# Kernel optimization log

Hardware: AMD Instinct MI355X
Metric: run time of the kernel (lower is better)

Reference implementation:

```python
import jax, jax.numpy as jnp
import numpy as np

DIM = 4096
N_HEADS = 32
N_KV_HEADS = 8
HEAD_DIM = 128
ROPE_THETA = 10000.0
REPEATS = N_HEADS // N_KV_HEADS
SCALE = HEAD_DIM ** -0.5


def rope(x, seq_len, offset):
    # x: [b, h, seq_len, head_dim]; faithful to source: cos/sin from cat((freqs,freqs)),
    # rotate built by interleaved pair swap then flatten.
    d = x.shape[-1]
    inv_freq = 1.0 / (ROPE_THETA ** (jnp.arange(0, d, 2, dtype=jnp.float32) / d))  # [d/2]
    t = jnp.arange(offset, offset + seq_len, dtype=jnp.float32)                    # [L]
    freqs = t[:, None] * inv_freq[None, :]                                         # [L, d/2]
    emb = jnp.concatenate([freqs, freqs], axis=-1)                                 # [L, d]
    cos_emb = jnp.cos(emb)
    sin_emb = jnp.sin(emb)
    x_even = x[..., 0::2]
    x_odd = x[..., 1::2]
    rotate_x = jnp.stack([-x_odd, x_even], axis=-1).reshape(x.shape)
    return x * cos_emb + rotate_x * sin_emb


def setup_inputs() -> dict:
    key = jax.random.key(0)
    k1, k2, k3, k4, k5 = jax.random.split(key, 5)
    b, l = 1, 2048
    s = 0.02
    x = jax.random.normal(k1, (b, l, DIM), dtype=jnp.float32)
    wq = jax.random.normal(k2, (DIM, N_HEADS * HEAD_DIM), dtype=jnp.float32) * s
    wk = jax.random.normal(k3, (DIM, N_KV_HEADS * HEAD_DIM), dtype=jnp.float32) * s
    wv = jax.random.normal(k4, (DIM, N_KV_HEADS * HEAD_DIM), dtype=jnp.float32) * s
    wo = jax.random.normal(k5, (N_HEADS * HEAD_DIM, DIM), dtype=jnp.float32) * s
    return {"x": x, "wq": wq, "wk": wk, "wv": wv, "wo": wo, "seq_len": l}


def reference(x, wq, wk, wv, wo, seq_len):
    b, l, _ = x.shape
    q = (x @ wq).reshape(b, l, N_HEADS, HEAD_DIM).transpose(0, 2, 1, 3)       # [b,H,l,d]
    k = (x @ wk).reshape(b, l, N_KV_HEADS, HEAD_DIM).transpose(0, 2, 1, 3)    # [b,Hk,l,d]
    v = (x @ wv).reshape(b, l, N_KV_HEADS, HEAD_DIM).transpose(0, 2, 1, 3)
    # repeat KV heads to match query heads (GQA)
    k = jnp.repeat(k, REPEATS, axis=1)   # [b,H,l,d]
    v = jnp.repeat(v, REPEATS, axis=1)
    offset = 0  # cache is None
    q = rope(q, seq_len, offset)
    k = rope(k, seq_len, offset)
    scores = jnp.einsum('bhid,bhjd->bhij', q * SCALE, k)
    scores = jax.nn.softmax(scores.astype(jnp.float32), axis=-1).astype(scores.dtype)
    out = jnp.einsum('bhij,bhjd->bhid', scores, v)
    out = out.transpose(0, 2, 1, 3).reshape(b, l, N_HEADS * HEAD_DIM)
    return out @ wo, (k, v)
```

## Files before the change

### kernel.cpp

```cpp
#include <hip/hip_runtime.h>
#include <cstdint>
#include <cstddef>

#define DIM 4096
#define SEQ 2048
#define NH 32
#define NKV 8
#define HD 128
#define QKVN 6144

typedef __bf16 bf16_t;
typedef __bf16 bf16x8 __attribute__((ext_vector_type(8)));
typedef __bf16 bf16x4 __attribute__((ext_vector_type(4)));
typedef __bf16 bf16x2 __attribute__((ext_vector_type(2)));
typedef float f32x4 __attribute__((ext_vector_type(4)));
typedef int int4v __attribute__((ext_vector_type(4)));

__device__ __forceinline__ f32x4 mfma16(bf16x8 a, bf16x8 b, f32x4 c) {
  return __builtin_amdgcn_mfma_f32_16x16x32_bf16(a, b, c, 0, 0, 0);
}

__device__ __forceinline__ void async16(const bf16_t* g, bf16_t* l) {
  __builtin_amdgcn_global_load_lds((__attribute__((address_space(1))) void*)g,
                                   (__attribute__((address_space(3))) void*)l,
                                   16, 0, 0);
}

__device__ __forceinline__ int pack2(float a, float b) {
  bf16x2 h = { (bf16_t)a, (bf16_t)b };
  return __builtin_bit_cast(int, h);
}

#define LGKM0() do { asm volatile("s_waitcnt lgkmcnt(0)" ::: "memory"); \
                     __builtin_amdgcn_sched_barrier(0); } while (0)
#define VMW4() do { asm volatile("s_waitcnt vmcnt(4)" ::: "memory"); \
                    __builtin_amdgcn_sched_barrier(0); } while (0)

__global__ void cast_x(const float* __restrict__ x, bf16_t* __restrict__ xb) {
  int i = blockIdx.x * 256 + threadIdx.x;
  const float4 v = ((const float4*)x)[i];
  bf16x4 o = { (bf16_t)v.x, (bf16_t)v.y, (bf16_t)v.z, (bf16_t)v.w };
  *(bf16x4*)(xb + (size_t)i * 4) = o;
}

__global__ void tcast(const float* __restrict__ src, bf16_t* __restrict__ dst,
                      int Ncols, int Kdim) {
  __shared__ float tile[32][33];
  int n0 = blockIdx.x * 32, k0 = blockIdx.y * 32;
  int tx = threadIdx.x, ty = threadIdx.y;
#pragma unroll
  for (int r = 0; r < 4; r++)
    tile[ty + 8 * r][tx] = src[(size_t)(k0 + ty + 8 * r) * Ncols + n0 + tx];
  __syncthreads();
#pragma unroll
  for (int r = 0; r < 4; r++)
    dst[(size_t)(n0 + ty + 8 * r) * Kdim + k0 + tx] = (bf16_t)tile[tx][ty + 8 * r];
}

__global__ __launch_bounds__(512) void gemm256(const bf16_t* __restrict__ A,
                                               const bf16_t* __restrict__ Bt,
                                               float* __restrict__ C,
                                               float* __restrict__ Cp,
                                               int M, int N, int K, int Kloc) {
  __shared__ bf16_t As[2][16384];
  __shared__ bf16_t Bs[2][16384];
  const int t = threadIdx.x;
  const int lane = t & 63;
  const int l15 = lane & 15, quad = lane >> 4;
  const int w = t >> 6, wm = w >> 2, wn = w & 3;

  const int gx = gridDim.x;
  const int nwg = gx * gridDim.y;
  const int id = blockIdx.y * gx + blockIdx.x;
  const int swz = (id & 7) * (nwg >> 3) + (id >> 3);
  const int bm = (swz / gx) * 256, bn = (swz % gx) * 256;
  const int kbase = blockIdx.z * Kloc;
  float* __restrict__ Cd = blockIdx.z ? Cp : C;

  const int srow = t >> 2;
  const int gcol = ((t & 3) ^ (srow & 3)) << 3;
  const bf16_t* gA = A + (size_t)(bm + srow) * K + kbase + gcol;
  const bf16_t* gB = Bt + (size_t)(bn + srow) * K + kbase + gcol;
  const int ldst = t * 8;

  const int fcol = ((quad ^ (l15 & 3)) << 3);

  f32x4 acc[8][4] = {};
  bf16x8 af[4], bfr[4][2];

  auto stKh = [&](int b2, int s, int kk) {
    async16(gA + kk + s * 32, &As[b2][s * 8192 + ldst]);
    async16(gA + (size_t)128 * K + kk + s * 32, &As[b2][s * 8192 + 4096 + ldst]);
    async16(gB + kk + s * 32, &Bs[b2][s * 8192 + ldst]);
    async16(gB + (size_t)128 * K + kk + s * 32, &Bs[b2][s * 8192 + 4096 + ldst]);
  };

  stKh(0, 0, 0);
  stKh(0, 1, 0);
  VMW4();
  __builtin_amdgcn_s_barrier();

  const int nkt = Kloc >> 6;
  for (int kt = 0; kt < nkt; ++kt) {
    const int b2 = kt & 1, bn2 = b2 ^ 1;
    const int kn = (kt + 1 == nkt) ? 0 : (kt + 1) << 6;

#pragma unroll
    for (int mi = 0; mi < 4; mi++)
      af[mi] = *(const bf16x8*)&As[b2][(wm * 128 + mi * 16 + l15) * 32 + fcol];
#pragma unroll
    for (int ni = 0; ni < 4; ni++)
      bfr[ni][0] = *(const bf16x8*)&Bs[b2][(wn * 64 + ni * 16 + l15) * 32 + fcol];
    stKh(bn2, 0, kn);
    __builtin_amdgcn_s_barrier();
    LGKM0();
    __builtin_amdgcn_s_setprio(1);
#pragma unroll
    for (int mi = 0; mi < 4; mi++)
#pragma unroll
      for (int ni = 0; ni < 4; ni++)
        acc[mi][ni] = mfma16(af[mi], bfr[ni][0], acc[mi][ni]);
    __builtin_amdgcn_s_setprio(0);
    VMW4();
    __builtin_amdgcn_s_barrier();

#pragma unroll
    for (int mi = 0; mi < 4; mi++)
      af[mi] = *(const bf16x8*)&As[b2][8192 + (wm * 128 + mi * 16 + l15) * 32 + fcol];
#pragma unroll
    for (int ni = 0; ni < 4; ni++)
      bfr[ni][1] = *(const bf16x8*)&Bs[b2][8192 + (wn * 64 + ni * 16 + l15) * 32 + fcol];
    stKh(bn2, 1, kn);
    __builtin_amdgcn_s_barrier();
    LGKM0();
    __builtin_amdgcn_s_setprio(1);
#pragma unroll
    for (int mi = 0; mi < 4; mi++)
#pragma unroll
      for (int ni = 0; ni < 4; ni++)
        acc[mi][ni] = mfma16(af[mi], bfr[ni][1], acc[mi][ni]);
    __builtin_amdgcn_s_setprio(0);
    __builtin_amdgcn_s_barrier();

#pragma unroll
    for (int mi = 0; mi < 4; mi++)
      af[mi] = *(const bf16x8*)&As[b2][(wm * 128 + 64 + mi * 16 + l15) * 32 + fcol];
    __builtin_amdgcn_s_barrier();
    LGKM0();
    __builtin_amdgcn_s_setprio(1);
#pragma unroll
    for (int mi = 0; mi < 4; mi++)
#pragma unroll
      for (int ni = 0; ni < 4; ni++)
        acc[mi + 4][ni] = mfma16(af[mi], bfr[ni][0], acc[mi + 4][ni]);
    __builtin_amdgcn_s_setprio(0);
    __builtin_amdgcn_s_barrier();

#pragma unroll
    for (int mi = 0; mi < 4; mi++)
      af[mi] = *(const bf16x8*)&As[b2][8192 + (wm * 128 + 64 + mi * 16 + l15) * 32 + fcol];
    __builtin_amdgcn_s_barrier();
    LGKM0();
    __builtin_amdgcn_s_setprio(1);
#pragma unroll
    for (int mi = 0; mi < 4; mi++)
#pragma unroll
      for (int ni = 0; ni < 4; ni++)
        acc[mi + 4][ni] = mfma16(af[mi], bfr[ni][1], acc[mi + 4][ni]);
    __builtin_amdgcn_s_setprio(0);
    VMW4();
    __builtin_amdgcn_s_barrier();
  }

#pragma unroll
  for (int m8 = 0; m8 < 8; m8++)
#pragma unroll
    for (int ni = 0; ni < 4; ni++) {
      size_t row = (size_t)bm + wm * 128 + (m8 >> 2) * 64 + (m8 & 3) * 16 + quad * 4;
      size_t col = (size_t)bn + wn * 64 + ni * 16 + l15;
#pragma unroll
      for (int r = 0; r < 4; r++)
        Cd[(row + r) * N + col] = acc[m8][ni][r];
    }
  asm volatile("s_waitcnt vmcnt(0)" ::: "memory");
}

__global__ void addf4(float* __restrict__ o, const float* __restrict__ p) {
  int i = blockIdx.x * 256 + threadIdx.x;
  float4 a = ((const float4*)o)[i];
  const float4 b = ((const float4*)p)[i];
  a.x += b.x; a.y += b.y; a.z += b.z; a.w += b.w;
  ((float4*)o)[i] = a;
}

__global__ void rope_scatter(const float* __restrict__ qkv, bf16_t* __restrict__ Qb,
                             bf16_t* __restrict__ Kb, bf16_t* __restrict__ Vt,
                             float* __restrict__ kOut, float* __restrict__ vOut) {
  int idx = blockIdx.x * 256 + threadIdx.x;
  int t = idx / 3072;
  int p = idx - t * 3072;
  const float NEG_L2T_64 = -0.20762050593046f;
  const float SS = 0.08838834764831845f * 1.4426950408889634f;
  if (p < 2048) {
    int hh = p >> 6, pr = p & 63;
    int d0 = pr << 1;
    const float* src = qkv + (size_t)t * QKVN + hh * HD + d0;
    float a = src[0], b = src[1];
    int j0 = d0 & 63, j1 = (d0 + 1) & 63;
    float th0 = (float)t * exp2f((float)j0 * NEG_L2T_64);
    float th1 = (float)t * exp2f((float)j1 * NEG_L2T_64);
    float o0 = (a * cosf(th0) - b * sinf(th0)) * SS;
    float o1 = (b * cosf(th1) + a * sinf(th1)) * SS;
    bf16_t* dst = Qb + ((size_t)hh * SEQ + t) * HD + d0;
    dst[0] = (bf16_t)o0;
    dst[1] = (bf16_t)o1;
  } else if (p < 2560) {
    int q2 = p - 2048;
    int kh = q2 >> 6, pr = q2 & 63;
    int d0 = pr << 1;
    const float* src = qkv + (size_t)t * QKVN + 4096 + kh * HD + d0;
    float a = src[0], b = src[1];
    int j0 = d0 & 63, j1 = (d0 + 1) & 63;
    float th0 = (float)t * exp2f((float)j0 * NEG_L2T_64);
    float th1 = (float)t * exp2f((float)j1 * NEG_L2T_64);
    float o0 = a * cosf(th0) - b * sinf(th0);
    float o1 = b * cosf(th1) + a * sinf(th1);
    bf16_t* dst = Kb + ((size_t)kh * SEQ + t) * HD + d0;
    dst[0] = (bf16_t)o0;
    dst[1] = (bf16_t)o1;
#pragma unroll
    for (int rep = 0; rep < 4; rep++) {
      float* kp = kOut + ((size_t)(kh * 4 + rep) * SEQ + t) * HD + d0;
      kp[0] = o0;
      kp[1] = o1;
    }
  } else {
    int q2 = p - 2560;
    int kh = q2 >> 6, pr = q2 & 63;
    int d0 = pr << 1;
    const float* src = qkv + (size_t)t * QKVN + 5120 + kh * HD + d0;
    float a = src[0], b = src[1];
#pragma unroll
    for (int rep = 0; rep < 4; rep++) {
      float* vp = vOut + ((size_t)(kh * 4 + rep) * SEQ + t) * HD + d0;
      vp[0] = a;
      vp[1] = b;
    }
    int tp = (t & ~31) + ((t & 12) << 1) + (t & 3) + ((t & 16) >> 2);
    Vt[((size_t)kh * HD + d0) * SEQ + tp] = (bf16_t)a;
    Vt[((size_t)kh * HD + d0 + 1) * SEQ + tp] = (bf16_t)b;
  }
}

__global__ __launch_bounds__(512, 2) void attn_kernel(const bf16_t* __restrict__ Qb,
                                                      const bf16_t* __restrict__ Kb,
                                                      const bf16_t* __restrict__ Vt,
                                                      bf16_t* __restrict__ AO) {
  __shared__ bf16_t Ks[2][8192];
  __shared__ bf16_t Vs[2][8192];
  const int h = blockIdx.y, kh = h >> 2;
  const int qbase = blockIdx.x * 256;
  const int w = threadIdx.x >> 6, lane = threadIdx.x & 63;
  const int l15 = lane & 15, quad = lane >> 4;
  const bf16_t* KbH = Kb + (size_t)kh * SEQ * HD;
  const bf16_t* VtH = Vt + (size_t)kh * HD * SEQ;

  bf16x8 qf[2][4];
#pragma unroll
  for (int nq = 0; nq < 2; nq++) {
    const bf16_t* qp = Qb + ((size_t)h * SEQ + qbase + w * 32 + nq * 16 + l15) * HD + quad * 8;
#pragma unroll
    for (int kc = 0; kc < 4; kc++) qf[nq][kc] = *(const bf16x8*)(qp + kc * 32);
  }

  f32x4 acc[8][2] = {};
  float rsum[2] = {0.f, 0.f};

  auto stage = [&](int buf, int kt0) {
    if (w < 4) {
      int kc = w;
#pragma unroll
      for (int kg = 0; kg < 4; kg++) {
        const bf16_t* g = KbH + (size_t)(kt0 + kg * 16 + (lane >> 2)) * HD + kc * 32 + (lane & 3) * 8;
        async16(g, &Ks[buf][kc * 2048 + kg * 512]);
      }
    } else {
      int vi = w - 4, kt = vi >> 1, dg0 = (vi & 1) * 4;
#pragma unroll
      for (int j = 0; j < 4; j++) {
        int dg = dg0 + j;
        const bf16_t* g = VtH + (size_t)(dg * 16 + (lane >> 2)) * SEQ + kt0 + kt * 32 + (lane & 3) * 8;
        async16(g, &Vs[buf][kt * 4096 + dg * 512]);
      }
    }
  };

  stage(0, 0);
  int buf = 0;

  for (int kt0 = 0; kt0 < SEQ; kt0 += 64, buf ^= 1) {
    __syncthreads();
    if (kt0 + 64 < SEQ) stage(buf ^ 1, kt0 + 64);

    f32x4 sacc[4][2] = {};
#pragma unroll
    for (int mi = 0; mi < 4; mi++)
#pragma unroll
      for (int kc = 0; kc < 4; kc++) {
        bf16x8 kf = *(const bf16x8*)(&Ks[buf][(kc * 64 + mi * 16 + l15) * 32 + quad * 8]);
#pragma unroll
        for (int nq = 0; nq < 2; nq++)
          sacc[mi][nq] = mfma16(kf, qf[nq][kc], sacc[mi][nq]);
      }

    int pk[4][2][2];
#pragma unroll
    for (int mi = 0; mi < 4; mi++)
#pragma unroll
      for (int nq = 0; nq < 2; nq++) {
        float p0 = exp2f(sacc[mi][nq][0]);
        float p1 = exp2f(sacc[mi][nq][1]);
        float p2 = exp2f(sacc[mi][nq][2]);
        float p3 = exp2f(sacc[mi][nq][3]);
        rsum[nq] += (p0 + p1) + (p2 + p3);
        pk[mi][nq][0] = pack2(p0, p1);
        pk[mi][nq][1] = pack2(p2, p3);
      }

#pragma unroll
    for (int kt = 0; kt < 2; kt++) {
#pragma unroll
      for (int nq = 0; nq < 2; nq++) {
        int4v dw;
        dw[0] = pk[2 * kt][nq][0];
        dw[1] = pk[2 * kt][nq][1];
        dw[2] = pk[2 * kt + 1][nq][0];
        dw[3] = pk[2 * kt + 1][nq][1];
        bf16x8 pf = __builtin_bit_cast(bf16x8, dw);
#pragma unroll
        for (int dt = 0; dt < 8; dt++) {
          bf16x8 vf = *(const bf16x8*)(&Vs[buf][(kt * 128 + dt * 16 + l15) * 32 + quad * 8]);
          acc[dt][nq] = mfma16(vf, pf, acc[dt][nq]);
        }
      }
    }
  }

#pragma unroll
  for (int nq = 0; nq < 2; nq++) {
    float rs = rsum[nq];
    rs += __shfl_xor(rs, 16);
    rs += __shfl_xor(rs, 32);
    float inv = 1.0f / rs;
    int q = qbase + w * 32 + nq * 16 + l15;
#pragma unroll
    for (int dt = 0; dt < 8; dt++) {
      bf16x4 o = { (bf16_t)(acc[dt][nq][0] * inv), (bf16_t)(acc[dt][nq][1] * inv),
                   (bf16_t)(acc[dt][nq][2] * inv), (bf16_t)(acc[dt][nq][3] * inv) };
      *(bf16x4*)(AO + (size_t)q * DIM + h * HD + dt * 16 + quad * 4) = o;
    }
  }
}

extern "C" void kernel_launch(void* const* d_in, const int* in_sizes, int n_in,
                              void* d_out, int out_size, void* d_ws, size_t ws_size,
                              hipStream_t stream) {
  const float* x = (const float*)d_in[0];
  const float* wq = (const float*)d_in[1];
  const float* wk = (const float*)d_in[2];
  const float* wv = (const float*)d_in[3];
  const float* wo = (const float*)d_in[4];
  float* out = (float*)d_out;
  float* kOut = out + (size_t)SEQ * DIM;
  float* vOut = kOut + (size_t)NH * SEQ * HD;

  char* ws = (char*)d_ws;
  bf16_t* Xb = (bf16_t*)ws;
  bf16_t* WT = (bf16_t*)(ws + 16777216);
  float* Cp1 = (float*)(ws + 16777216);
  float* QKV = (float*)(ws + 67108864);
  bf16_t* WoT = (bf16_t*)(ws + 67108864);
  bf16_t* Qb = (bf16_t*)(ws + 117440512);
  bf16_t* Kb = (bf16_t*)(ws + 134217728);
  bf16_t* Vt = (bf16_t*)(ws + 138412032);
  bf16_t* AO = Xb;

  dim3 tb(32, 8);
  cast_x<<<8192, 256, 0, stream>>>(x, Xb);
  tcast<<<dim3(128, 128), tb, 0, stream>>>(wq, WT, 4096, 4096);
  tcast<<<dim3(32, 128), tb, 0, stream>>>(wk, WT + (size_t)4096 * 4096, 1024, 4096);
  tcast<<<dim3(32, 128), tb, 0, stream>>>(wv, WT + (size_t)5120 * 4096, 1024, 4096);
  gemm256<<<dim3(24, 8, 1), 512, 0, stream>>>(Xb, WT, QKV, nullptr, 2048, 6144, 4096, 4096);
  rope_scatter<<<24576, 256, 0, stream>>>(QKV, Qb, Kb, Vt, kOut, vOut);
  tcast<<<dim3(128, 128), tb, 0, stream>>>(wo, WoT, 4096, 4096);
  attn_kernel<<<dim3(8, 32), 512, 0, stream>>>(Qb, Kb, Vt, AO);
  gemm256<<<dim3(16, 8, 2), 512, 0, stream>>>(AO, WoT, out, Cp1, 2048, 4096, 4096, 2048);
  addf4<<<8192, 256, 0, stream>>>(out, Cp1);
}
```

Measured before the change: 578.8 us.

## Restructure GEMM LDS tiles to full 64-wide K rows with 8-way XOR swizzle

Changes the shared-memory tile layout from two 32-column K-halves to a single 64-column row per tile, staged with one batch of eight async loads per k-step and an 8-way XOR swizzle. Both halves of the B fragments are loaded at once, and the vmcnt waits are retimed so half of the next stage is waited on mid-iteration. The aim is wider contiguous global reads (128B per row) and fewer barrier and wait points per iteration. The risk is that the new swizzle or the partial-wait timing adds bank conflicts or exposes load latency.

```diff
diff --git a/kernel.cpp b/kernel.cpp
--- a/kernel.cpp
+++ b/kernel.cpp
@@ -33,8 +33,12 @@
 
 #define LGKM0() do { asm volatile("s_waitcnt lgkmcnt(0)" ::: "memory"); \
                      __builtin_amdgcn_sched_barrier(0); } while (0)
-#define VMW4() do { asm volatile("s_waitcnt vmcnt(4)" ::: "memory"); \
-                    __builtin_amdgcn_sched_barrier(0); } while (0)
+
+template <int N> __device__ __forceinline__ void vmw() {
+  if constexpr (N == 2) asm volatile("s_waitcnt vmcnt(2)" ::: "memory");
+  else if constexpr (N == 8) asm volatile("s_waitcnt vmcnt(8)" ::: "memory");
+  __builtin_amdgcn_sched_barrier(0);
+}
 
 __global__ void cast_x(const float* __restrict__ x, bf16_t* __restrict__ xb) {
   int i = blockIdx.x * 256 + threadIdx.x;
@@ -77,27 +81,31 @@
   const int kbase = blockIdx.z * Kloc;
   float* __restrict__ Cd = blockIdx.z ? Cp : C;
 
-  const int srow = t >> 2;
-  const int gcol = ((t & 3) ^ (srow & 3)) << 3;
-  const bf16_t* gA = A + (size_t)(bm + srow) * K + kbase + gcol;
-  const bf16_t* gB = Bt + (size_t)(bn + srow) * K + kbase + gcol;
+  const int srow = t >> 3;
+  const int scol = ((t & 7) ^ (srow & 7)) << 3;
+  const bf16_t* gA = A + (size_t)(bm + srow) * K + kbase + scol;
+  const bf16_t* gB = Bt + (size_t)(bn + srow) * K + kbase + scol;
   const int ldst = t * 8;
 
-  const int fcol = ((quad ^ (l15 & 3)) << 3);
+  const int g0 = ((quad ^ (l15 & 7)) << 3);
+  const int g1 = (((4 | quad) ^ (l15 & 7)) << 3);
 
   f32x4 acc[8][4] = {};
   bf16x8 af[4], bfr[4][2];
 
-  auto stKh = [&](int b2, int s, int kk) {
-    async16(gA + kk + s * 32, &As[b2][s * 8192 + ldst]);
-    async16(gA + (size_t)128 * K + kk + s * 32, &As[b2][s * 8192 + 4096 + ldst]);
-    async16(gB + kk + s * 32, &Bs[b2][s * 8192 + ldst]);
-    async16(gB + (size_t)128 * K + kk + s * 32, &Bs[b2][s * 8192 + 4096 + ldst]);
+  auto stage = [&](int b2, int kk) {
+    async16(gA + kk, &As[b2][ldst]);
+    async16(gA + (size_t)128 * K + kk, &As[b2][8192 + ldst]);
+    async16(gB + kk, &Bs[b2][ldst]);
+    async16(gB + (size_t)64 * K + kk, &Bs[b2][4096 + ldst]);
+    async16(gB + (size_t)128 * K + kk, &Bs[b2][8192 + ldst]);
+    async16(gB + (size_t)192 * K + kk, &Bs[b2][12288 + ldst]);
+    async16(gA + (size_t)64 * K + kk, &As[b2][4096 + ldst]);
+    async16(gA + (size_t)192 * K + kk, &As[b2][12288 + ldst]);
   };
 
-  stKh(0, 0, 0);
-  stKh(0, 1, 0);
-  VMW4();
+  stage(0, 0);
+  vmw<2>();
   __builtin_amdgcn_s_barrier();
 
   const int nkt = Kloc >> 6;
@@ -107,11 +115,13 @@
 
 #pragma unroll
     for (int mi = 0; mi < 4; mi++)
-      af[mi] = *(const bf16x8*)&As[b2][(wm * 128 + mi * 16 + l15) * 32 + fcol];
-#pragma unroll
-    for (int ni = 0; ni < 4; ni++)
-      bfr[ni][0] = *(const bf16x8*)&Bs[b2][(wn * 64 + ni * 16 + l15) * 32 + fcol];
-    stKh(bn2, 0, kn);
+      af[mi] = *(const bf16x8*)&As[b2][(wm * 128 + mi * 16 + l15) * 64 + g0];
+#pragma unroll
+    for (int ni = 0; ni < 4; ni++) {
+      bfr[ni][0] = *(const bf16x8*)&Bs[b2][(wn * 64 + ni * 16 + l15) * 64 + g0];
+      bfr[ni][1] = *(const bf16x8*)&Bs[b2][(wn * 64 + ni * 16 + l15) * 64 + g1];
+    }
+    stage(bn2, kn);
     __builtin_amdgcn_s_barrier();
     LGKM0();
     __builtin_amdgcn_s_setprio(1);
@@ -121,16 +131,11 @@
       for (int ni = 0; ni < 4; ni++)
         acc[mi][ni] = mfma16(af[mi], bfr[ni][0], acc[mi][ni]);
     __builtin_amdgcn_s_setprio(0);
-    VMW4();
-    __builtin_amdgcn_s_barrier();
-
-#pragma unroll
-    for (int mi = 0; mi < 4; mi++)
-      af[mi] = *(const bf16x8*)&As[b2][8192 + (wm * 128 + mi * 16 + l15) * 32 + fcol];
-#pragma unroll
-    for (int ni = 0; ni < 4; ni++)
-      bfr[ni][1] = *(const bf16x8*)&Bs[b2][8192 + (wn * 64 + ni * 16 + l15) * 32 + fcol];
-    stKh(bn2, 1, kn);
+    __builtin_amdgcn_s_barrier();
+
+#pragma unroll
+    for (int mi = 0; mi < 4; mi++)
+      af[mi] = *(const bf16x8*)&As[b2][(wm * 128 + mi * 16 + l15) * 64 + g1];
     __builtin_amdgcn_s_barrier();
     LGKM0();
     __builtin_amdgcn_s_setprio(1);
@@ -140,11 +145,12 @@
       for (int ni = 0; ni < 4; ni++)
         acc[mi][ni] = mfma16(af[mi], bfr[ni][1], acc[mi][ni]);
     __builtin_amdgcn_s_setprio(0);
-    __builtin_amdgcn_s_barrier();
-
-#pragma unroll
-    for (int mi = 0; mi < 4; mi++)
-      af[mi] = *(const bf16x8*)&As[b2][(wm * 128 + 64 + mi * 16 + l15) * 32 + fcol];
+    vmw<8>();
+    __builtin_amdgcn_s_barrier();
+
+#pragma unroll
+    for (int mi = 0; mi < 4; mi++)
+      af[mi] = *(const bf16x8*)&As[b2][(wm * 128 + 64 + mi * 16 + l15) * 64 + g0];
     __builtin_amdgcn_s_barrier();
     LGKM0();
     __builtin_amdgcn_s_setprio(1);
@@ -158,7 +164,7 @@
 
 #pragma unroll
     for (int mi = 0; mi < 4; mi++)
-      af[mi] = *(const bf16x8*)&As[b2][8192 + (wm * 128 + 64 + mi * 16 + l15) * 32 + fcol];
+      af[mi] = *(const bf16x8*)&As[b2][(wm * 128 + 64 + mi * 16 + l15) * 64 + g1];
     __builtin_amdgcn_s_barrier();
     LGKM0();
     __builtin_amdgcn_s_setprio(1);
@@ -168,7 +174,7 @@
       for (int ni = 0; ni < 4; ni++)
         acc[mi + 4][ni] = mfma16(af[mi], bfr[ni][1], acc[mi + 4][ni]);
     __builtin_amdgcn_s_setprio(0);
-    VMW4();
+    vmw<2>();
     __builtin_amdgcn_s_barrier();
   }
 
```

Result: no change. 578.0 us (-0.1%).
